# Kernel tuning notes

Hardware: AMD Instinct MI355X
Metric: run time of the kernel (lower is better)

The kernel has to match this reference:

```python
import jax, jax.numpy as jnp
import numpy as np

N, C, H, W, P = 64, 256, 64, 64, 1024
GAMMA = 1.0  # __init__ arg


def setup_inputs() -> dict:
    key = jax.random.key(0)
    k1, k2, k3 = jax.random.split(key, 3)
    inp = jax.random.normal(k1, (N, C, H, W), dtype=jnp.float32)
    # absolute pixel coords (y, x) in [0, H-1] x [0, W-1]
    point = jax.random.uniform(k2, (N, P, 2), dtype=jnp.float32) * jnp.array([H - 1, W - 1], dtype=jnp.float32)
    offset = jax.random.normal(k3, (N, P, 2), dtype=jnp.float32) * 0.5
    return {"input": inp, "point": point, "offset": offset}


def _bilinear_sample(inp, pos):
    """inp: [n,c,h,w]; pos: [n,p,2] (y,x) absolute pixel coords -> [n,p,c].
    Out-of-bounds corners contribute zero (matches CUDA bilinear with zero padding)."""
    n, c, h, w = inp.shape
    y = pos[..., 0]
    x = pos[..., 1]
    y0f = jnp.floor(y)
    x0f = jnp.floor(x)
    ly = y - y0f  # fractional parts
    lx = x - x0f
    hy = 1.0 - ly
    hx = 1.0 - lx
    y0 = y0f.astype(jnp.int32)
    x0 = x0f.astype(jnp.int32)

    feat = jnp.transpose(inp, (0, 2, 3, 1))  # [n,h,w,c] for contiguous channel gather
    b = jnp.arange(n)[:, None]  # [n,1] broadcast against [n,p]

    def gather(yi, xi):
        valid = (yi >= 0) & (yi < h) & (xi >= 0) & (xi < w)  # [n,p]
        yc = jnp.clip(yi, 0, h - 1)
        xc = jnp.clip(xi, 0, w - 1)
        v = feat[b, yc, xc]  # [n,p,c]
        return v * valid[..., None].astype(v.dtype)

    v00 = gather(y0, x0)
    v01 = gather(y0, x0 + 1)
    v10 = gather(y0 + 1, x0)
    v11 = gather(y0 + 1, x0 + 1)

    w00 = (hy * hx)[..., None]
    w01 = (hy * lx)[..., None]
    w10 = (ly * hx)[..., None]
    w11 = (ly * lx)[..., None]
    return v00 * w00 + v01 * w01 + v10 * w10 + v11 * w11


def reference(input, point, offset):
    pos = point + GAMMA * offset  # [n,p,2] (y,x)
    return _bilinear_sample(input, pos)
```

## Files before the change

kernel.cpp:

```cpp
#include <hip/hip_runtime.h>

constexpr int N = 64, C = 256, H = 64, W = 64, P = 1024;
constexpr int PLANE   = H * W;
constexpr int GC      = 8;
constexpr int THREADS = 1024;
constexpr int NBUF    = 4;

typedef float v4f __attribute__((ext_vector_type(4)));

__device__ __forceinline__ void stage_plane(const float* __restrict__ src,
                                            float* __restrict__ dst, int t) {
    const int tb = t & ~63;
    __builtin_amdgcn_global_load_lds(
        (const __attribute__((address_space(1))) void*)(src + (t << 2)),
        (__attribute__((address_space(3))) void*)(dst + (tb << 2)),
        16, 0, 0);
}

__global__ __launch_bounds__(THREADS, 2) void progressive_sample_kernel(
    const float* __restrict__ inp,
    const float* __restrict__ point,
    const float* __restrict__ offset,
    float* __restrict__ out)
{
    __shared__ __align__(16) float buf[NBUF][PLANE];

    const int b = blockIdx.x;
    const int n = b >> 5;
    const int g = b & 31;
    const int t = threadIdx.x;
    const int chan0 = g * GC;

    const float* src = inp + ((size_t)n * C + chan0) * PLANE;

    const float2 pt2 = ((const float2*)point )[((size_t)n << 10) + t];
    const float2 of2 = ((const float2*)offset)[((size_t)n << 10) + t];
    stage_plane(src,             buf[0], t);
    stage_plane(src + PLANE,     buf[1], t);
    stage_plane(src + 2 * PLANE, buf[2], t);

    const float y = pt2.x + of2.x;
    const float x = pt2.y + of2.y;
    const float y0f = floorf(y), x0f = floorf(x);
    const float ly = y - y0f, lx = x - x0f;
    const float hy = 1.0f - ly, hx = 1.0f - lx;
    const int y0 = (int)y0f, x0 = (int)x0f, y1 = y0 + 1, x1 = x0 + 1;
    const bool vy0 = (unsigned)y0 < (unsigned)H, vy1 = (unsigned)y1 < (unsigned)H;
    const bool vx0 = (unsigned)x0 < (unsigned)W, vx1 = (unsigned)x1 < (unsigned)W;
    const int yc0 = min(max(y0, 0), H - 1), yc1 = min(max(y1, 0), H - 1);
    const int xc0 = min(max(x0, 0), W - 1), xc1 = min(max(x1, 0), W - 1);
    const int i00 = yc0 * W + xc0, i01 = yc0 * W + xc1;
    const int i10 = yc1 * W + xc0, i11 = yc1 * W + xc1;
    const float w00 = (vy0 && vx0) ? hy * hx : 0.0f;
    const float w01 = (vy0 && vx1) ? hy * lx : 0.0f;
    const float w10 = (vy1 && vx0) ? ly * hx : 0.0f;
    const float w11 = (vy1 && vx1) ? ly * lx : 0.0f;

    float acc[GC];

    #pragma unroll
    for (int k = 0; k < GC; ++k) {
        if (k <= GC - 3) {
            asm volatile("s_waitcnt vmcnt(2)" ::: "memory");
        } else if (k == GC - 2) {
            asm volatile("s_waitcnt vmcnt(1)" ::: "memory");
        } else {
            asm volatile("s_waitcnt vmcnt(0)" ::: "memory");
        }
        __builtin_amdgcn_sched_barrier(0);
        __builtin_amdgcn_s_barrier();
        __builtin_amdgcn_sched_barrier(0);

        if (k + 3 < GC)
            stage_plane(src + (size_t)(k + 3) * PLANE, buf[(k + 3) & 3], t);

        const float* __restrict__ bk = buf[k & 3];
        acc[k] = bk[i00] * w00 + bk[i01] * w01
               + bk[i10] * w10 + bk[i11] * w11;

        asm volatile("s_waitcnt lgkmcnt(0)" ::: "memory");
        __builtin_amdgcn_sched_barrier(0);
    }

    float* o = out + (((size_t)n << 10) + t) * C + chan0;
    v4f v0 = { acc[0], acc[1], acc[2], acc[3] };
    v4f v1 = { acc[4], acc[5], acc[6], acc[7] };
    *(v4f*)o       = v0;
    *(v4f*)(o + 4) = v1;
}

extern "C" void kernel_launch(void* const* d_in, const int* in_sizes, int n_in,
                              void* d_out, int out_size, void* d_ws, size_t ws_size,
                              hipStream_t stream) {
    const float* inp    = (const float*)d_in[0];
    const float* point  = (const float*)d_in[1];
    const float* offset = (const float*)d_in[2];
    float* out = (float*)d_out;

    progressive_sample_kernel<<<N * (C / GC), THREADS, 0, stream>>>(
        inp, point, offset, out);
}
```

Before: 79.32 us.

## Stage planes through registers with triple-buffered LDS and 16 channels per block

Replaces the direct global-to-LDS async loads with ordinary float4 global loads into registers, which are then written to a 3-deep LDS ring one iteration ahead. The channels per block go from 8 to 16, halving the grid and the per-block point setup and doubling the contiguous output write per thread. The change relies on register staging and the compiler's vmcnt handling instead of explicit waitcnt on global_load_lds. The launch_bounds minimum-blocks hint goes from 2 to 8, which is probably not reachable with 1024-thread blocks and 48KB of LDS each. Fewer, longer blocks may reduce occupancy and tail balance.

```diff
diff --git a/kernel.cpp b/kernel.cpp
--- a/kernel.cpp
+++ b/kernel.cpp
@@ -2,53 +2,44 @@
 
 constexpr int N = 64, C = 256, H = 64, W = 64, P = 1024;
 constexpr int PLANE   = H * W;
-constexpr int GC      = 8;
+constexpr int GC      = 16;
 constexpr int THREADS = 1024;
-constexpr int NBUF    = 4;
+constexpr int NBUF    = 3;
 
 typedef float v4f __attribute__((ext_vector_type(4)));
 
-__device__ __forceinline__ void stage_plane(const float* __restrict__ src,
-                                            float* __restrict__ dst, int t) {
-    const int tb = t & ~63;
-    __builtin_amdgcn_global_load_lds(
-        (const __attribute__((address_space(1))) void*)(src + (t << 2)),
-        (__attribute__((address_space(3))) void*)(dst + (tb << 2)),
-        16, 0, 0);
-}
-
-__global__ __launch_bounds__(THREADS, 2) void progressive_sample_kernel(
+__global__ __launch_bounds__(THREADS, 8) void progressive_sample_kernel(
     const float* __restrict__ inp,
     const float* __restrict__ point,
     const float* __restrict__ offset,
     float* __restrict__ out)
 {
     __shared__ __align__(16) float buf[NBUF][PLANE];
+    const int b  = blockIdx.x;
+    const int n  = b >> 4;
+    const int gq = b & 15;
+    const int t  = threadIdx.x;
+    const int c0 = gq * GC;
 
-    const int b = blockIdx.x;
-    const int n = b >> 5;
-    const int g = b & 31;
-    const int t = threadIdx.x;
-    const int chan0 = g * GC;
-
-    const float* src = inp + ((size_t)n * C + chan0) * PLANE;
+    const float4* __restrict__ srcv =
+        (const float4*)(inp + ((size_t)n * C + c0) * PLANE);
 
     const float2 pt2 = ((const float2*)point )[((size_t)n << 10) + t];
     const float2 of2 = ((const float2*)offset)[((size_t)n << 10) + t];
-    stage_plane(src,             buf[0], t);
-    stage_plane(src + PLANE,     buf[1], t);
-    stage_plane(src + 2 * PLANE, buf[2], t);
+    float4 g0t = srcv[t];
+    float4 g[2];
+    g[1] = srcv[1024 + t];
 
     const float y = pt2.x + of2.x;
     const float x = pt2.y + of2.y;
     const float y0f = floorf(y), x0f = floorf(x);
     const float ly = y - y0f, lx = x - x0f;
     const float hy = 1.0f - ly, hx = 1.0f - lx;
-    const int y0 = (int)y0f, x0 = (int)x0f, y1 = y0 + 1, x1 = x0 + 1;
+    const int y0 = (int)y0f, xi0 = (int)x0f, y1 = y0 + 1, xi1 = xi0 + 1;
     const bool vy0 = (unsigned)y0 < (unsigned)H, vy1 = (unsigned)y1 < (unsigned)H;
-    const bool vx0 = (unsigned)x0 < (unsigned)W, vx1 = (unsigned)x1 < (unsigned)W;
+    const bool vx0 = (unsigned)xi0 < (unsigned)W, vx1 = (unsigned)xi1 < (unsigned)W;
     const int yc0 = min(max(y0, 0), H - 1), yc1 = min(max(y1, 0), H - 1);
-    const int xc0 = min(max(x0, 0), W - 1), xc1 = min(max(x1, 0), W - 1);
+    const int xc0 = min(max(xi0, 0), W - 1), xc1 = min(max(xi1, 0), W - 1);
     const int i00 = yc0 * W + xc0, i01 = yc0 * W + xc1;
     const int i10 = yc1 * W + xc0, i11 = yc1 * W + xc1;
     const float w00 = (vy0 && vx0) ? hy * hx : 0.0f;
@@ -56,37 +47,37 @@
     const float w10 = (vy1 && vx0) ? ly * hx : 0.0f;
     const float w11 = (vy1 && vx1) ? ly * lx : 0.0f;
 
+    *(float4*)&buf[0][t << 2] = g0t;
+    asm volatile("s_waitcnt lgkmcnt(0)" ::: "memory");
+    __builtin_amdgcn_sched_barrier(0);
+
     float acc[GC];
 
     #pragma unroll
     for (int k = 0; k < GC; ++k) {
-        if (k <= GC - 3) {
-            asm volatile("s_waitcnt vmcnt(2)" ::: "memory");
-        } else if (k == GC - 2) {
-            asm volatile("s_waitcnt vmcnt(1)" ::: "memory");
-        } else {
-            asm volatile("s_waitcnt vmcnt(0)" ::: "memory");
-        }
-        __builtin_amdgcn_sched_barrier(0);
         __builtin_amdgcn_s_barrier();
         __builtin_amdgcn_sched_barrier(0);
 
-        if (k + 3 < GC)
-            stage_plane(src + (size_t)(k + 3) * PLANE, buf[(k + 3) & 3], t);
+        if (k + 2 < GC)
+            g[k & 1] = srcv[(k + 2) * 1024 + t];
 
-        const float* __restrict__ bk = buf[k & 3];
+        const float* __restrict__ bk = &buf[k % 3][0];
         acc[k] = bk[i00] * w00 + bk[i01] * w01
                + bk[i10] * w10 + bk[i11] * w11;
+
+        if (k + 1 < GC)
+            *(float4*)&buf[(k + 1) % 3][t << 2] = g[(k + 1) & 1];
 
         asm volatile("s_waitcnt lgkmcnt(0)" ::: "memory");
         __builtin_amdgcn_sched_barrier(0);
     }
 
-    float* o = out + (((size_t)n << 10) + t) * C + chan0;
-    v4f v0 = { acc[0], acc[1], acc[2], acc[3] };
-    v4f v1 = { acc[4], acc[5], acc[6], acc[7] };
-    *(v4f*)o       = v0;
-    *(v4f*)(o + 4) = v1;
+    float* o = out + (((size_t)n << 10) + t) * C + c0;
+    #pragma unroll
+    for (int q = 0; q < 4; ++q) {
+        v4f v = { acc[4*q+0], acc[4*q+1], acc[4*q+2], acc[4*q+3] };
+        *(v4f*)(o + 4 * q) = v;
+    }
 }
 
 extern "C" void kernel_launch(void* const* d_in, const int* in_sizes, int n_in,
```

New measurement: 113.8 us. 43.4% more time.

## Process 32 channels per block with streamed LDS pipeline and periodic stores

Applied to the files above, without the earlier changes.

Each block now walks 32 channel planes instead of 8 through the same 4-buffer global-to-LDS pipeline, storing output in chunks of 8 channels as it goes. This amortises the per-block prologue (point/offset loads, weight computation, pipeline fill and drain) over more planes and cuts the grid from 2048 to 512 blocks. The vmcnt waits are adjusted so they also account for the outstanding output stores. The risk is fewer blocks in flight: 512 blocks of 1024 threads may underfill the GPU and hurt latency hiding. The launch-bounds hint is also raised.

```diff
diff --git a/kernel.cpp b/kernel.cpp
--- a/kernel.cpp
+++ b/kernel.cpp
@@ -2,9 +2,9 @@
 
 constexpr int N = 64, C = 256, H = 64, W = 64, P = 1024;
 constexpr int PLANE   = H * W;
-constexpr int GC      = 8;
 constexpr int THREADS = 1024;
 constexpr int NBUF    = 4;
+constexpr int PHASES  = 32;
 
 typedef float v4f __attribute__((ext_vector_type(4)));
 
@@ -17,7 +17,7 @@
         16, 0, 0);
 }
 
-__global__ __launch_bounds__(THREADS, 2) void progressive_sample_kernel(
+__global__ __launch_bounds__(THREADS, 8) void progressive_sample_kernel(
     const float* __restrict__ inp,
     const float* __restrict__ point,
     const float* __restrict__ offset,
@@ -25,13 +25,13 @@
 {
     __shared__ __align__(16) float buf[NBUF][PLANE];
 
-    const int b = blockIdx.x;
-    const int n = b >> 5;
-    const int g = b & 31;
-    const int t = threadIdx.x;
-    const int chan0 = g * GC;
+    const int b    = blockIdx.x;
+    const int n    = b >> 3;
+    const int setg = b & 7;
+    const int t    = threadIdx.x;
+    const int cb   = setg << 5;
 
-    const float* src = inp + ((size_t)n * C + chan0) * PLANE;
+    const float* src = inp + ((size_t)n * C + cb) * PLANE;
 
     const float2 pt2 = ((const float2*)point )[((size_t)n << 10) + t];
     const float2 of2 = ((const float2*)offset)[((size_t)n << 10) + t];
@@ -44,11 +44,11 @@
     const float y0f = floorf(y), x0f = floorf(x);
     const float ly = y - y0f, lx = x - x0f;
     const float hy = 1.0f - ly, hx = 1.0f - lx;
-    const int y0 = (int)y0f, x0 = (int)x0f, y1 = y0 + 1, x1 = x0 + 1;
+    const int y0 = (int)y0f, xi0 = (int)x0f, y1 = y0 + 1, xi1 = xi0 + 1;
     const bool vy0 = (unsigned)y0 < (unsigned)H, vy1 = (unsigned)y1 < (unsigned)H;
-    const bool vx0 = (unsigned)x0 < (unsigned)W, vx1 = (unsigned)x1 < (unsigned)W;
+    const bool vx0 = (unsigned)xi0 < (unsigned)W, vx1 = (unsigned)xi1 < (unsigned)W;
     const int yc0 = min(max(y0, 0), H - 1), yc1 = min(max(y1, 0), H - 1);
-    const int xc0 = min(max(x0, 0), W - 1), xc1 = min(max(x1, 0), W - 1);
+    const int xc0 = min(max(xi0, 0), W - 1), xc1 = min(max(xi1, 0), W - 1);
     const int i00 = yc0 * W + xc0, i01 = yc0 * W + xc1;
     const int i10 = yc1 * W + xc0, i11 = yc1 * W + xc1;
     const float w00 = (vy0 && vx0) ? hy * hx : 0.0f;
@@ -56,37 +56,41 @@
     const float w10 = (vy1 && vx0) ? ly * hx : 0.0f;
     const float w11 = (vy1 && vx1) ? ly * lx : 0.0f;
 
-    float acc[GC];
+    float* const obase = out + (((size_t)n << 10) + t) * C + cb;
+
+    float acc[8];
 
     #pragma unroll
-    for (int k = 0; k < GC; ++k) {
-        if (k <= GC - 3) {
-            asm volatile("s_waitcnt vmcnt(2)" ::: "memory");
-        } else if (k == GC - 2) {
-            asm volatile("s_waitcnt vmcnt(1)" ::: "memory");
-        } else {
-            asm volatile("s_waitcnt vmcnt(0)" ::: "memory");
-        }
+    for (int m = 0; m < PHASES; ++m) {
+        const int Wm = (m >= 8 && (m & 7) <= 2) ? 4
+                     : (m == PHASES - 2) ? 1
+                     : (m == PHASES - 1) ? 0 : 2;
+        if (Wm == 4)      asm volatile("s_waitcnt vmcnt(4)" ::: "memory");
+        else if (Wm == 2) asm volatile("s_waitcnt vmcnt(2)" ::: "memory");
+        else if (Wm == 1) asm volatile("s_waitcnt vmcnt(1)" ::: "memory");
+        else              asm volatile("s_waitcnt vmcnt(0)" ::: "memory");
         __builtin_amdgcn_sched_barrier(0);
         __builtin_amdgcn_s_barrier();
         __builtin_amdgcn_sched_barrier(0);
 
-        if (k + 3 < GC)
-            stage_plane(src + (size_t)(k + 3) * PLANE, buf[(k + 3) & 3], t);
+        if (m + 3 < PHASES)
+            stage_plane(src + (size_t)(m + 3) * PLANE, buf[(m + 3) & 3], t);
 
-        const float* __restrict__ bk = buf[k & 3];
-        acc[k] = bk[i00] * w00 + bk[i01] * w01
-               + bk[i10] * w10 + bk[i11] * w11;
+        const float* __restrict__ bk = buf[m & 3];
+        acc[m & 7] = bk[i00] * w00 + bk[i01] * w01
+                   + bk[i10] * w10 + bk[i11] * w11;
 
         asm volatile("s_waitcnt lgkmcnt(0)" ::: "memory");
         __builtin_amdgcn_sched_barrier(0);
+
+        if ((m & 7) == 7) {
+            float* o = obase + ((m >> 3) << 3);
+            v4f lo = { acc[0], acc[1], acc[2], acc[3] };
+            v4f hi = { acc[4], acc[5], acc[6], acc[7] };
+            *(v4f*)o       = lo;
+            *(v4f*)(o + 4) = hi;
+        }
     }
-
-    float* o = out + (((size_t)n << 10) + t) * C + chan0;
-    v4f v0 = { acc[0], acc[1], acc[2], acc[3] };
-    v4f v1 = { acc[4], acc[5], acc[6], acc[7] };
-    *(v4f*)o       = v0;
-    *(v4f*)(o + 4) = v1;
 }
 
 extern "C" void kernel_launch(void* const* d_in, const int* in_sizes, int n_in,
@@ -97,6 +101,6 @@
     const float* offset = (const float*)d_in[2];
     float* out = (float*)d_out;
 
-    progressive_sample_kernel<<<N * (C / GC), THREADS, 0, stream>>>(
+    progressive_sample_kernel<<<N * 8, THREADS, 0, stream>>>(
         inp, point, offset, out);
 }
```

New measurement: 84.23 us. +6.2%, slower.
